# Kernel optimization log

Hardware: AMD Instinct MI355X
Metric: run time of the kernel (lower is better)

Reference implementation:

```python
import jax, jax.numpy as jnp
import numpy as np

B, P, D, A = 256, 196, 512, 512

def setup_inputs() -> dict:
    key = jax.random.key(0)
    ks = jax.random.split(key, 12)
    sc = 1.0 / np.sqrt(D)
    sa = 1.0 / np.sqrt(A)
    return {
        "encoder_out": jax.random.normal(ks[0], (B, P, D), jnp.float32),
        "decoder_hidden": jax.random.normal(ks[1], (B, D), jnp.float32),
        "st": jax.random.normal(ks[2], (B, D), jnp.float32),
        "Wv": jax.random.normal(ks[3], (D, A), jnp.float32) * sc,
        "bv": jnp.zeros((A,), jnp.float32),
        "Wh": jax.random.normal(ks[4], (D, A), jnp.float32) * sc,
        "bh": jnp.zeros((A,), jnp.float32),
        "Ws": jax.random.normal(ks[5], (D, A), jnp.float32) * sc,
        "bs": jnp.zeros((A,), jnp.float32),
        "Wav": jax.random.normal(ks[6], (A,), jnp.float32) * sa,
        "bav": jnp.zeros((), jnp.float32),
        "Was": jax.random.normal(ks[7], (A,), jnp.float32) * sa,
        "bas": jnp.zeros((), jnp.float32),
    }

def reference(encoder_out, decoder_hidden, st, Wv, bv, Wh, bh, Ws, bs, Wav, bav, Was, bas):
    # hidden: (B, A)
    hidden = decoder_hidden @ Wh + bh
    # v: (B, P, A)
    v = jnp.einsum('bpd,da->bpa', encoder_out, Wv) + bv
    # z_t: (B, P) -- additive attention scores over pixels
    z_t = jnp.einsum('bpa,a->bp', jnp.tanh(v + hidden[:, None, :]), Wav) + bav
    alpha_t = jax.nn.softmax(z_t, axis=1)
    # c_t: (B, D) -- attention-weighted encoding
    c_t = jnp.einsum('bpd,bp->bd', encoder_out, alpha_t)
    # sentinel branch: s (B, A), s_att (B, 1)
    s = st @ Ws + bs
    s_att = jnp.tanh(s + hidden) @ Was + bas  # (B,)
    z_t_extended = jnp.concatenate([z_t, s_att[:, None]], axis=1)  # (B, P+1)
    alpha_t_hat = jax.nn.softmax(z_t_extended, axis=1)
    beta_t = alpha_t_hat[:, -1:]  # (B, 1)
    c_hat_t = beta_t * st + (1.0 - beta_t) * c_t
    return (c_hat_t, alpha_t, beta_t)
```

## Files before the change

### kernel.cpp

```cpp
#include <hip/hip_runtime.h>
#include <hip/hip_bf16.h>
#include <cstdint>

#define B_ 256
#define P_ 196
#define D_ 512
#define A_ 512

#define OUT_CHAT  0
#define OUT_ALPHA (B_*D_)
#define OUT_BETA  (B_*D_ + B_*P_)

typedef unsigned short ushort_t;
typedef uint32_t u32;
typedef uint64_t u64;
typedef __attribute__((ext_vector_type(8))) __bf16 bf16x8;
typedef __attribute__((ext_vector_type(4))) float f32x4;

__device__ __forceinline__ ushort_t f2bf(float f) {
    union { float f; u32 i; } v; v.f = f;
    u32 r = (v.i + 0x7fffu + ((v.i >> 16) & 1u)) >> 16;
    return (ushort_t)r;
}
__device__ __forceinline__ float bfbits2f(u32 lo16) {
    union { u32 i; float f; } v; v.i = lo16 << 16; return v.f;
}
__device__ __forceinline__ u32 cvt2bf(float x, float y) {
    union { __hip_bfloat162 h; u32 u; } v;
    v.h = __float22bfloat162_rn(make_float2(x, y));
    return v.u;
}
__device__ __forceinline__ float tanh_fast(float x) {
    float e = __expf(2.0f * x);
    return 1.0f - 2.0f / (e + 1.0f);
}
__device__ __forceinline__ void async_load16(const ushort_t* g, ushort_t* l) {
    __builtin_amdgcn_global_load_lds(
        (const __attribute__((address_space(1))) unsigned int*)g,
        (__attribute__((address_space(3))) unsigned int*)l, 16, 0, 0);
}
__device__ __forceinline__ void fma8(float ap, uint4 v, float ac[8]) {
    ac[0] = fmaf(ap, bfbits2f(v.x & 0xffffu), ac[0]);
    ac[1] = fmaf(ap, bfbits2f(v.x >> 16),     ac[1]);
    ac[2] = fmaf(ap, bfbits2f(v.y & 0xffffu), ac[2]);
    ac[3] = fmaf(ap, bfbits2f(v.y >> 16),     ac[3]);
    ac[4] = fmaf(ap, bfbits2f(v.z & 0xffffu), ac[4]);
    ac[5] = fmaf(ap, bfbits2f(v.z >> 16),     ac[5]);
    ac[6] = fmaf(ap, bfbits2f(v.w & 0xffffu), ac[6]);
    ac[7] = fmaf(ap, bfbits2f(v.w >> 16),     ac[7]);
}

__global__ __launch_bounds__(256) void k_prep(
    const float* __restrict__ E, const float* __restrict__ dh,
    const float* __restrict__ st,
    const float* __restrict__ Wv, const float* __restrict__ Wh,
    const float* __restrict__ Ws,
    ushort_t* __restrict__ Ebf, ushort_t* __restrict__ dhbf,
    ushort_t* __restrict__ stbf,
    ushort_t* __restrict__ WvT, ushort_t* __restrict__ WhT,
    ushort_t* __restrict__ WsT)
{
    __shared__ ushort_t tile[32][33];
    int bx = blockIdx.x;
    if (bx < 12544) {
        size_t i0 = (size_t)bx * 512 + threadIdx.x;
        const float4* src = (const float4*)E;
        u64* dst = (u64*)Ebf;
        float4 v0 = src[i0];
        float4 v1 = src[i0 + 256];
        dst[i0]       = (u64)cvt2bf(v0.x, v0.y) | ((u64)cvt2bf(v0.z, v0.w) << 32);
        dst[i0 + 256] = (u64)cvt2bf(v1.x, v1.y) | ((u64)cvt2bf(v1.z, v1.w) << 32);
    } else if (bx < 12672) {
        int gid = (bx - 12544) * 256 + threadIdx.x;
        float4 dv = ((const float4*)dh)[gid];
        float4 sv = ((const float4*)st)[gid];
        ((u64*)dhbf)[gid] = (u64)cvt2bf(dv.x, dv.y) | ((u64)cvt2bf(dv.z, dv.w) << 32);
        ((u64*)stbf)[gid] = (u64)cvt2bf(sv.x, sv.y) | ((u64)cvt2bf(sv.z, sv.w) << 32);
    } else {
        int idx = bx - 12672;
        int z   = idx >> 8;
        int rem = idx & 255;
        int tby = rem >> 4, tbx = rem & 15;
        const float* W  = (z == 0) ? Wv  : (z == 1) ? Wh  : Ws;
        ushort_t*    WT = (z == 0) ? WvT : (z == 1) ? WhT : WsT;
        int t = threadIdx.x, r = t >> 5, c = t & 31;
#pragma unroll
        for (int i = 0; i < 4; ++i) {
            int row = r + 8 * i;
            tile[row][c] = f2bf(W[(size_t)(tby * 32 + row) * A_ + tbx * 32 + c]);
        }
        __syncthreads();
#pragma unroll
        for (int i = 0; i < 4; ++i) {
            int row = r + 8 * i;
            WT[(size_t)(tbx * 32 + row) * D_ + tby * 32 + c] = tile[c][row];
        }
    }
}

#define PADK 72

__global__ __launch_bounds__(256) void k1_mfma(
    const ushort_t* __restrict__ dhbf, const ushort_t* __restrict__ stbf,
    const ushort_t* __restrict__ WhT,  const ushort_t* __restrict__ WsT,
    const float* __restrict__ bh, const float* __restrict__ bs,
    float* __restrict__ hidden_ws, float* __restrict__ s_ws)
{
    __shared__ ushort_t As[128 * PADK];
    __shared__ ushort_t Bs[128 * PADK];

    int mat = blockIdx.z;
    const ushort_t* Abf = mat ? stbf : dhbf;
    const ushort_t* WT  = mat ? WsT  : WhT;
    const float*    bia = mat ? bs   : bh;
    float*          outp = mat ? s_ws : hidden_ws;

    int tid = threadIdx.x;
    int m0 = blockIdx.y * 128;
    int n0 = blockIdx.x * 128;

    int lane = tid & 63, w = tid >> 6;
    int wm = w & 1, wn = w >> 1;
    int col = lane & 15, q = lane >> 4;

    f32x4 acc[4][4];
#pragma unroll
    for (int tm = 0; tm < 4; ++tm)
#pragma unroll
        for (int tn = 0; tn < 4; ++tn)
            acc[tm][tn] = (f32x4){0.f, 0.f, 0.f, 0.f};

    const ushort_t* arow = As + (wm * 64 + col) * PADK + q * 8;
    const ushort_t* brow = Bs + (wn * 64 + col) * PADK + q * 8;

    int sr = tid >> 3, sc = tid & 7;
    for (int kt = 0; kt < D_ / 64; ++kt) {
#pragma unroll
        for (int i = 0; i < 4; ++i) {
            int row = sr + i * 32;
            *(uint4*)(As + row * PADK + sc * 8) =
                *(const uint4*)(Abf + (size_t)(m0 + row) * D_ + kt * 64 + sc * 8);
            *(uint4*)(Bs + row * PADK + sc * 8) =
                *(const uint4*)(WT + (size_t)(n0 + row) * D_ + kt * 64 + sc * 8);
        }
        __syncthreads();
#pragma unroll
        for (int ks = 0; ks < 2; ++ks) {
            bf16x8 afr[4];
#pragma unroll
            for (int tm = 0; tm < 4; ++tm)
                afr[tm] = *(const bf16x8*)(arow + tm * 16 * PADK + ks * 32);
#pragma unroll
            for (int tn = 0; tn < 4; ++tn) {
                bf16x8 bfr = *(const bf16x8*)(brow + tn * 16 * PADK + ks * 32);
#pragma unroll
                for (int tm = 0; tm < 4; ++tm)
                    acc[tm][tn] = __builtin_amdgcn_mfma_f32_16x16x32_bf16(
                        afr[tm], bfr, acc[tm][tn], 0, 0, 0);
            }
        }
        __syncthreads();
    }

#pragma unroll
    for (int tm = 0; tm < 4; ++tm)
#pragma unroll
        for (int r = 0; r < 4; ++r) {
            int b = m0 + wm * 64 + tm * 16 + q * 4 + r;
#pragma unroll
            for (int tn = 0; tn < 4; ++tn) {
                int n = n0 + wn * 64 + tn * 16 + col;
                outp[(size_t)b * A_ + n] = acc[tm][tn][r] + bia[n];
            }
        }
}

#define BM 128
#define BN 256
#define BKk 64
__global__ __launch_bounds__(256, 3) void k2_z_bf(
    const ushort_t* __restrict__ Ebf, const ushort_t* __restrict__ WvT,
    const float* __restrict__ hidden_ws, const float* __restrict__ bv,
    const float* __restrict__ Wav, float* __restrict__ z2_ws)
{
    __shared__ ushort_t As[BM * BKk];
    __shared__ ushort_t Bs[BN * BKk];
    __shared__ float hv_s[2][BN];
    __shared__ float wav_s[BN];
    __shared__ float zpart[2][BM];

    int tid = threadIdx.x;
    int bx  = blockIdx.x;
    int m_idx = ((bx >> 4) << 3) + (bx & 7);
    int half  = (bx >> 3) & 1;
    int m0  = m_idx * BM;
    int n0  = half * BN;
    int b0  = m0 / P_;
    int b1  = (m0 + BM - 1) / P_;

    {
        int a = n0 + tid;
        float bva = bv[a];
        hv_s[0][tid] = hidden_ws[(size_t)b0 * A_ + a] + bva;
        hv_s[1][tid] = hidden_ws[(size_t)b1 * A_ + a] + bva;
        wav_s[tid]   = Wav[a];
    }

    int lane = tid & 63, w = tid >> 6;
    int wm = w & 1, wn = w >> 1;
    int col = lane & 15, q = lane >> 4;

    f32x4 acc[4][8];
#pragma unroll
    for (int tm = 0; tm < 4; ++tm)
#pragma unroll
        for (int tn = 0; tn < 8; ++tn)
            acc[tm][tn] = (f32x4){0.f, 0.f, 0.f, 0.f};

    int srow = tid >> 3, spos = tid & 7;
    int gch  = spos ^ (srow & 7);
    const ushort_t* agb = Ebf + (size_t)(m0 + srow) * D_ + gch * 8;
    const ushort_t* bgb = WvT + (size_t)(n0 + srow) * D_ + gch * 8;
    ushort_t* alb = As + tid * 8;
    ushort_t* blb = Bs + tid * 8;

    int fx = col & 7;

    for (int kt = 0; kt < D_ / BKk; ++kt) {
#pragma unroll
        for (int i = 0; i < 4; ++i)
            async_load16(agb + (size_t)i * 32 * D_ + kt * BKk, alb + i * 2048);
#pragma unroll
        for (int i = 0; i < 8; ++i)
            async_load16(bgb + (size_t)i * 32 * D_ + kt * BKk, blb + i * 2048);
        __syncthreads();
#pragma unroll
        for (int ks = 0; ks < 2; ++ks) {
            bf16x8 afr[4];
#pragma unroll
            for (int tm = 0; tm < 4; ++tm)
                afr[tm] = *(const bf16x8*)(As + (wm * 64 + tm * 16 + col) * BKk
                                              + (((ks * 4 + q) ^ fx) * 8));
#pragma unroll
            for (int tn = 0; tn < 8; ++tn) {
                bf16x8 bfr = *(const bf16x8*)(Bs + (wn * 128 + tn * 16 + col) * BKk
                                                 + (((ks * 4 + q) ^ fx) * 8));
#pragma unroll
                for (int tm = 0; tm < 4; ++tm)
                    acc[tm][tn] = __builtin_amdgcn_mfma_f32_16x16x32_bf16(
                        afr[tm], bfr, acc[tm][tn], 0, 0, 0);
            }
        }
        __syncthreads();
    }

#pragma unroll
    for (int tm = 0; tm < 4; ++tm) {
#pragma unroll
        for (int r = 0; r < 4; ++r) {
            int row = wm * 64 + tm * 16 + q * 4 + r;
            int m   = m0 + row;
            int bsel = (m / P_) - b0;
            float zr = 0.f;
#pragma unroll
            for (int tn = 0; tn < 8; ++tn) {
                int nl = wn * 128 + tn * 16 + col;
                zr += wav_s[nl] * tanh_fast(acc[tm][tn][r] + hv_s[bsel][nl]);
            }
#pragma unroll
            for (int msk = 1; msk < 16; msk <<= 1)
                zr += __shfl_xor(zr, msk, 64);
            if (col == 0) zpart[wn][row] = zr;
        }
    }
    __syncthreads();
    if (tid < BM)
        z2_ws[(size_t)half * (B_ * P_) + m0 + tid] =
            zpart[0][tid] + zpart[1][tid];
}

__global__ __launch_bounds__(512) void k34_softmax_ct(
    const ushort_t* __restrict__ Ebf, const float* __restrict__ st,
    const float* __restrict__ z2_ws, const float* __restrict__ hidden_ws,
    const float* __restrict__ s_ws, const float* __restrict__ Was,
    const float* __restrict__ bas, const float* __restrict__ bav,
    float* __restrict__ out)
{
    __shared__ float red[8];
    __shared__ float al[P_];
    __shared__ float acc_s[8][516];
    __shared__ float bm_s, bl_s, sa_s;

    int b = blockIdx.x, t = threadIdx.x;
    int lane = t & 63, w = t >> 6;

    float part = Was[t] * tanh_fast(s_ws[(size_t)b * A_ + t]
                                  + hidden_ws[(size_t)b * A_ + t]);
#pragma unroll
    for (int o = 32; o >= 1; o >>= 1) part += __shfl_down(part, o, 64);
    if (lane == 0) red[w] = part;
    __syncthreads();
    if (t == 0) {
        float s = 0.f;
#pragma unroll
        for (int i = 0; i < 8; ++i) s += red[i];
        sa_s = s + bas[0];
    }
    __syncthreads();

    float zv = (t < P_) ? (z2_ws[(size_t)b * P_ + t]
                         + z2_ws[(size_t)(B_ * P_) + (size_t)b * P_ + t] + bav[0])
                        : -1e30f;
    float m = zv;
#pragma unroll
    for (int o = 32; o >= 1; o >>= 1) m = fmaxf(m, __shfl_xor(m, o, 64));
    if (lane == 0) red[w] = m;
    __syncthreads();
    if (t == 0) {
        float mm = red[0];
#pragma unroll
        for (int i = 1; i < 8; ++i) mm = fmaxf(mm, red[i]);
        bm_s = mm;
    }
    __syncthreads();
    float m1 = bm_s;
    float e = (t < P_) ? __expf(zv - m1) : 0.f;
    float s = e;
#pragma unroll
    for (int o = 32; o >= 1; o >>= 1) s += __shfl_xor(s, o, 64);
    if (lane == 0) red[w] = s;
    __syncthreads();
    if (t == 0) {
        float ss = 0.f;
#pragma unroll
        for (int i = 0; i < 8; ++i) ss += red[i];
        bl_s = ss;
    }
    __syncthreads();
    float l1 = bl_s;
    if (t < P_) {
        float alpha = e / l1;
        al[t] = alpha;
        out[OUT_ALPHA + (size_t)b * P_ + t] = alpha;
    }
    float sa = sa_s;
    float m2 = fmaxf(m1, sa);
    float eb2 = __expf(sa - m2);
    float l2 = __expf(m1 - m2) * l1 + eb2;
    float beta = eb2 / l2;
    if (t == 0) out[OUT_BETA + b] = beta;
    __syncthreads();

    float ac[8] = {0.f, 0.f, 0.f, 0.f, 0.f, 0.f, 0.f, 0.f};
    const uint4* eb = (const uint4*)(Ebf + (size_t)b * P_ * D_);
#pragma unroll 4
    for (int i = 0; i < 24; ++i) {
        int pp = w + 8 * i;
        uint4 v = eb[(size_t)pp * (D_ / 8) + lane];
        fma8(al[pp], v, ac);
    }
    if (w < P_ - 192) {
        int pp = 192 + w;
        uint4 v = eb[(size_t)pp * (D_ / 8) + lane];
        fma8(al[pp], v, ac);
    }
#pragma unroll
    for (int j = 0; j < 8; ++j) acc_s[w][lane * 8 + j] = ac[j];
    __syncthreads();
    float c = 0.f;
#pragma unroll
    for (int g = 0; g < 8; ++g) c += acc_s[g][t];
    float sv = st[(size_t)b * D_ + t];
    out[OUT_CHAT + (size_t)b * D_ + t] = beta * sv + (1.f - beta) * c;
}

extern "C" void kernel_launch(void* const* d_in, const int* in_sizes, int n_in,
                              void* d_out, int out_size, void* d_ws, size_t ws_size,
                              hipStream_t stream)
{
    (void)in_sizes; (void)n_in; (void)out_size; (void)ws_size;
    const float* E   = (const float*)d_in[0];
    const float* dh  = (const float*)d_in[1];
    const float* st  = (const float*)d_in[2];
    const float* Wv  = (const float*)d_in[3];
    const float* bv  = (const float*)d_in[4];
    const float* Wh  = (const float*)d_in[5];
    const float* bh  = (const float*)d_in[6];
    const float* Ws  = (const float*)d_in[7];
    const float* bs  = (const float*)d_in[8];
    const float* Wav = (const float*)d_in[9];
    const float* bav = (const float*)d_in[10];
    const float* Was = (const float*)d_in[11];
    const float* bas = (const float*)d_in[12];
    float* out = (float*)d_out;

    char* ws = (char*)d_ws;
    ushort_t* WvT     = (ushort_t*)(ws);
    ushort_t* WhT     = (ushort_t*)(ws + 524288);
    ushort_t* WsT     = (ushort_t*)(ws + 1048576);
    float*    z2_w    = (float*)(ws + 1572864);
    ushort_t* dhbf    = (ushort_t*)(ws + 1974272);
    ushort_t* stbf    = (ushort_t*)(ws + 2236416);
    float*    hidden_w= (float*)(ws + 2498560);
    float*    s_w     = (float*)(ws + 3022848);
    ushort_t* Ebf     = (ushort_t*)(ws + 3547136);

    k_prep<<<12544 + 128 + 768, 256, 0, stream>>>(E, dh, st, Wv, Wh, Ws,
                                                  Ebf, dhbf, stbf, WvT, WhT, WsT);
    k1_mfma<<<dim3(4, 2, 2), 256, 0, stream>>>(dhbf, stbf, WhT, WsT, bh, bs,
                                               hidden_w, s_w);
    k2_z_bf<<<784, 256, 0, stream>>>(Ebf, WvT, hidden_w, bv, Wav, z2_w);
    k34_softmax_ct<<<256, 512, 0, stream>>>(Ebf, st, z2_w, hidden_w, s_w,
                                            Was, bas, bav, out);
}
```

Measured before the change: 251.3 us.

## Double-buffer k2 GEMM tiles, shrink N tile, interleave z partial sums

The score GEMM kernel now double-buffers its A and B shared-memory tiles, so the next K slice is prefetched while the current one is multiplied. The N tile shrinks from 256 to 128, giving a 2D grid of four N-blocks per M tile with fewer accumulators per thread, and occupancy is lowered to 2 blocks per CU. Partial z sums are stored interleaved, four per row, so the softmax kernel reads them with one float4 load. The z workspace now reuses the WhT/WsT region, which is safe only because k1 has finished reading those buffers before k2 runs.

```diff
diff --git a/kernel.cpp b/kernel.cpp
--- a/kernel.cpp
+++ b/kernel.cpp
@@ -176,29 +176,26 @@
 }
 
 #define BM 128
-#define BN 256
+#define BN2 128
 #define BKk 64
-__global__ __launch_bounds__(256, 3) void k2_z_bf(
+__global__ __launch_bounds__(256, 2) void k2_z_bf(
     const ushort_t* __restrict__ Ebf, const ushort_t* __restrict__ WvT,
     const float* __restrict__ hidden_ws, const float* __restrict__ bv,
     const float* __restrict__ Wav, float* __restrict__ z2_ws)
 {
-    __shared__ ushort_t As[BM * BKk];
-    __shared__ ushort_t Bs[BN * BKk];
-    __shared__ float hv_s[2][BN];
-    __shared__ float wav_s[BN];
+    __shared__ ushort_t As[2][BM * BKk];
+    __shared__ ushort_t Bs[2][BN2 * BKk];
+    __shared__ float hv_s[2][BN2];
+    __shared__ float wav_s[BN2];
     __shared__ float zpart[2][BM];
 
     int tid = threadIdx.x;
-    int bx  = blockIdx.x;
-    int m_idx = ((bx >> 4) << 3) + (bx & 7);
-    int half  = (bx >> 3) & 1;
-    int m0  = m_idx * BM;
-    int n0  = half * BN;
+    int m0  = blockIdx.x * BM;
+    int n0  = blockIdx.y * BN2;
     int b0  = m0 / P_;
     int b1  = (m0 + BM - 1) / P_;
 
-    {
+    if (tid < BN2) {
         int a = n0 + tid;
         float bva = bv[a];
         hv_s[0][tid] = hidden_ws[(size_t)b0 * A_ + a] + bva;
@@ -210,40 +207,50 @@
     int wm = w & 1, wn = w >> 1;
     int col = lane & 15, q = lane >> 4;
 
-    f32x4 acc[4][8];
+    f32x4 acc[4][4];
 #pragma unroll
     for (int tm = 0; tm < 4; ++tm)
 #pragma unroll
-        for (int tn = 0; tn < 8; ++tn)
+        for (int tn = 0; tn < 4; ++tn)
             acc[tm][tn] = (f32x4){0.f, 0.f, 0.f, 0.f};
 
     int srow = tid >> 3, spos = tid & 7;
     int gch  = spos ^ (srow & 7);
     const ushort_t* agb = Ebf + (size_t)(m0 + srow) * D_ + gch * 8;
     const ushort_t* bgb = WvT + (size_t)(n0 + srow) * D_ + gch * 8;
-    ushort_t* alb = As + tid * 8;
-    ushort_t* blb = Bs + tid * 8;
 
     int fx = col & 7;
 
+#pragma unroll
+    for (int i = 0; i < 4; ++i) {
+        async_load16(agb + (size_t)i * 32 * D_, &As[0][0] + tid * 8 + i * 2048);
+        async_load16(bgb + (size_t)i * 32 * D_, &Bs[0][0] + tid * 8 + i * 2048);
+    }
+    __syncthreads();
+
     for (int kt = 0; kt < D_ / BKk; ++kt) {
-#pragma unroll
-        for (int i = 0; i < 4; ++i)
-            async_load16(agb + (size_t)i * 32 * D_ + kt * BKk, alb + i * 2048);
-#pragma unroll
-        for (int i = 0; i < 8; ++i)
-            async_load16(bgb + (size_t)i * 32 * D_ + kt * BKk, blb + i * 2048);
-        __syncthreads();
+        int cur = kt & 1;
+        if (kt < D_ / BKk - 1) {
+#pragma unroll
+            for (int i = 0; i < 4; ++i) {
+                async_load16(agb + (size_t)i * 32 * D_ + (kt + 1) * BKk,
+                             &As[cur ^ 1][0] + tid * 8 + i * 2048);
+                async_load16(bgb + (size_t)i * 32 * D_ + (kt + 1) * BKk,
+                             &Bs[cur ^ 1][0] + tid * 8 + i * 2048);
+            }
+        }
+        const ushort_t* Ab = &As[cur][0];
+        const ushort_t* Bb = &Bs[cur][0];
 #pragma unroll
         for (int ks = 0; ks < 2; ++ks) {
             bf16x8 afr[4];
 #pragma unroll
             for (int tm = 0; tm < 4; ++tm)
-                afr[tm] = *(const bf16x8*)(As + (wm * 64 + tm * 16 + col) * BKk
+                afr[tm] = *(const bf16x8*)(Ab + (wm * 64 + tm * 16 + col) * BKk
                                               + (((ks * 4 + q) ^ fx) * 8));
 #pragma unroll
-            for (int tn = 0; tn < 8; ++tn) {
-                bf16x8 bfr = *(const bf16x8*)(Bs + (wn * 128 + tn * 16 + col) * BKk
+            for (int tn = 0; tn < 4; ++tn) {
+                bf16x8 bfr = *(const bf16x8*)(Bb + (wn * 64 + tn * 16 + col) * BKk
                                                  + (((ks * 4 + q) ^ fx) * 8));
 #pragma unroll
                 for (int tm = 0; tm < 4; ++tm)
@@ -263,8 +270,8 @@
             int bsel = (m / P_) - b0;
             float zr = 0.f;
 #pragma unroll
-            for (int tn = 0; tn < 8; ++tn) {
-                int nl = wn * 128 + tn * 16 + col;
+            for (int tn = 0; tn < 4; ++tn) {
+                int nl = wn * 64 + tn * 16 + col;
                 zr += wav_s[nl] * tanh_fast(acc[tm][tn][r] + hv_s[bsel][nl]);
             }
 #pragma unroll
@@ -275,7 +282,7 @@
     }
     __syncthreads();
     if (tid < BM)
-        z2_ws[(size_t)half * (B_ * P_) + m0 + tid] =
+        z2_ws[(size_t)(m0 + tid) * 4 + blockIdx.y] =
             zpart[0][tid] + zpart[1][tid];
 }
 
@@ -308,9 +315,11 @@
     }
     __syncthreads();
 
-    float zv = (t < P_) ? (z2_ws[(size_t)b * P_ + t]
-                         + z2_ws[(size_t)(B_ * P_) + (size_t)b * P_ + t] + bav[0])
-                        : -1e30f;
+    float zv = -1e30f;
+    if (t < P_) {
+        float4 z4 = ((const float4*)z2_ws)[(size_t)b * P_ + t];
+        zv = z4.x + z4.y + z4.z + z4.w + bav[0];
+    }
     float m = zv;
 #pragma unroll
     for (int o = 32; o >= 1; o >>= 1) m = fmaxf(m, __shfl_xor(m, o, 64));
@@ -398,18 +407,19 @@
     ushort_t* WvT     = (ushort_t*)(ws);
     ushort_t* WhT     = (ushort_t*)(ws + 524288);
     ushort_t* WsT     = (ushort_t*)(ws + 1048576);
-    float*    z2_w    = (float*)(ws + 1572864);
-    ushort_t* dhbf    = (ushort_t*)(ws + 1974272);
-    ushort_t* stbf    = (ushort_t*)(ws + 2236416);
-    float*    hidden_w= (float*)(ws + 2498560);
-    float*    s_w     = (float*)(ws + 3022848);
-    ushort_t* Ebf     = (ushort_t*)(ws + 3547136);
+    float*    z2_w    = (float*)(ws + 524288);
+    ushort_t* dhbf    = (ushort_t*)(ws + 1572864);
+    ushort_t* stbf    = (ushort_t*)(ws + 1835008);
+    float*    hidden_w= (float*)(ws + 2097152);
+    float*    s_w     = (float*)(ws + 2621440);
+    ushort_t* Ebf     = (ushort_t*)(ws + 3145728);
 
     k_prep<<<12544 + 128 + 768, 256, 0, stream>>>(E, dh, st, Wv, Wh, Ws,
                                                   Ebf, dhbf, stbf, WvT, WhT, WsT);
     k1_mfma<<<dim3(4, 2, 2), 256, 0, stream>>>(dhbf, stbf, WhT, WsT, bh, bs,
                                                hidden_w, s_w);
-    k2_z_bf<<<784, 256, 0, stream>>>(Ebf, WvT, hidden_w, bv, Wav, z2_w);
+    k2_z_bf<<<dim3((B_ * P_) / BM, A_ / BN2), 256, 0, stream>>>(
+        Ebf, WvT, hidden_w, bv, Wav, z2_w);
     k34_softmax_ct<<<256, 512, 0, stream>>>(Ebf, st, z2_w, hidden_w, s_w,
                                             Was, bas, bav, out);
 }
```

Result: no change. 256.3 us (+2.0%).

## Stage full-K activation tile in LDS and stream Wv from global per warp

Applied to the files above, without the earlier changes.

The attention-score GEMM kernel is restructured so each block owns 64 rows of the flattened (B·P) dimension across all 512 attention columns. The whole K=512 slice of the bf16 encoder tile is loaded into LDS once, with a single barrier. Each warp then reads its 128 Wv columns straight from global/L2 instead of from a shared tile. This drops the per-K-step barriers and the split of z into two halves, so the softmax kernel reads one z buffer. In exchange, every block re-reads the whole of Wv from L2 without LDS reuse. The large LDS footprint also lowers occupancy, and the workspace is repacked so z aliases the already-consumed WhT region.

```diff
diff --git a/kernel.cpp b/kernel.cpp
--- a/kernel.cpp
+++ b/kernel.cpp
@@ -175,40 +175,45 @@
         }
 }
 
-#define BM 128
-#define BN 256
-#define BKk 64
-__global__ __launch_bounds__(256, 3) void k2_z_bf(
+#define BM3 64
+__global__ __launch_bounds__(256, 2) void k2_z_bf(
     const ushort_t* __restrict__ Ebf, const ushort_t* __restrict__ WvT,
     const float* __restrict__ hidden_ws, const float* __restrict__ bv,
-    const float* __restrict__ Wav, float* __restrict__ z2_ws)
+    const float* __restrict__ Wav, float* __restrict__ z_ws)
 {
-    __shared__ ushort_t As[BM * BKk];
-    __shared__ ushort_t Bs[BN * BKk];
-    __shared__ float hv_s[2][BN];
-    __shared__ float wav_s[BN];
-    __shared__ float zpart[2][BM];
+    __shared__ ushort_t As[BM3 * 512];
+    __shared__ float hv_s[2][A_];
+    __shared__ float wav_s[A_];
+    __shared__ float zpart[4][BM3];
 
     int tid = threadIdx.x;
-    int bx  = blockIdx.x;
-    int m_idx = ((bx >> 4) << 3) + (bx & 7);
-    int half  = (bx >> 3) & 1;
-    int m0  = m_idx * BM;
-    int n0  = half * BN;
-    int b0  = m0 / P_;
-    int b1  = (m0 + BM - 1) / P_;
+    int m0 = blockIdx.x * BM3;
+    int b0 = m0 / P_, b1 = (m0 + BM3 - 1) / P_;
+
+#pragma unroll
+    for (int j = 0; j < 2; ++j) {
+        int a = j * 256 + tid;
+        float bva = bv[a];
+        hv_s[0][a] = hidden_ws[(size_t)b0 * A_ + a] + bva;
+        hv_s[1][a] = hidden_ws[(size_t)b1 * A_ + a] + bva;
+        wav_s[a]   = Wav[a];
+    }
+
+    int lane = tid & 63, w = tid >> 6;
+    int col = lane & 15, q = lane >> 4;
 
     {
-        int a = n0 + tid;
-        float bva = bv[a];
-        hv_s[0][tid] = hidden_ws[(size_t)b0 * A_ + a] + bva;
-        hv_s[1][tid] = hidden_ws[(size_t)b1 * A_ + a] + bva;
-        wav_s[tid]   = Wav[a];
-    }
-
-    int lane = tid & 63, w = tid >> 6;
-    int wm = w & 1, wn = w >> 1;
-    int col = lane & 15, q = lane >> 4;
+        int r0 = tid >> 6, sc = tid & 63;
+#pragma unroll
+        for (int i = 0; i < 16; ++i) {
+            int row  = i * 4 + r0;
+            int slot = sc ^ (row & 7);
+            async_load16(Ebf + (size_t)(m0 + row) * D_ + slot * 8,
+                         As + i * 2048 + tid * 8);
+        }
+    }
+    asm volatile("s_waitcnt vmcnt(0)" ::: "memory");
+    __builtin_amdgcn_s_barrier();
 
     f32x4 acc[4][8];
 #pragma unroll
@@ -217,71 +222,53 @@
         for (int tn = 0; tn < 8; ++tn)
             acc[tm][tn] = (f32x4){0.f, 0.f, 0.f, 0.f};
 
-    int srow = tid >> 3, spos = tid & 7;
-    int gch  = spos ^ (srow & 7);
-    const ushort_t* agb = Ebf + (size_t)(m0 + srow) * D_ + gch * 8;
-    const ushort_t* bgb = WvT + (size_t)(n0 + srow) * D_ + gch * 8;
-    ushort_t* alb = As + tid * 8;
-    ushort_t* blb = Bs + tid * 8;
-
     int fx = col & 7;
-
-    for (int kt = 0; kt < D_ / BKk; ++kt) {
-#pragma unroll
-        for (int i = 0; i < 4; ++i)
-            async_load16(agb + (size_t)i * 32 * D_ + kt * BKk, alb + i * 2048);
-#pragma unroll
-        for (int i = 0; i < 8; ++i)
-            async_load16(bgb + (size_t)i * 32 * D_ + kt * BKk, blb + i * 2048);
-        __syncthreads();
-#pragma unroll
-        for (int ks = 0; ks < 2; ++ks) {
-            bf16x8 afr[4];
+    const ushort_t* bgp = WvT + (size_t)(w * 128 + col) * D_ + q * 8;
+
+#pragma unroll
+    for (int k32 = 0; k32 < 16; ++k32) {
+        bf16x8 afr[4];
+#pragma unroll
+        for (int tm = 0; tm < 4; ++tm)
+            afr[tm] = *(const bf16x8*)(As + (tm * 16 + col) * 512
+                                          + (((k32 * 4 + q) ^ fx) * 8));
+#pragma unroll
+        for (int tn = 0; tn < 8; ++tn) {
+            bf16x8 bfr = *(const bf16x8*)(bgp + (size_t)tn * 16 * D_ + k32 * 32);
 #pragma unroll
             for (int tm = 0; tm < 4; ++tm)
-                afr[tm] = *(const bf16x8*)(As + (wm * 64 + tm * 16 + col) * BKk
-                                              + (((ks * 4 + q) ^ fx) * 8));
+                acc[tm][tn] = __builtin_amdgcn_mfma_f32_16x16x32_bf16(
+                    afr[tm], bfr, acc[tm][tn], 0, 0, 0);
+        }
+    }
+
+#pragma unroll
+    for (int tm = 0; tm < 4; ++tm) {
+#pragma unroll
+        for (int r = 0; r < 4; ++r) {
+            int row = tm * 16 + q * 4 + r;
+            int bsel = ((m0 + row) / P_) - b0;
+            float zr = 0.f;
 #pragma unroll
             for (int tn = 0; tn < 8; ++tn) {
-                bf16x8 bfr = *(const bf16x8*)(Bs + (wn * 128 + tn * 16 + col) * BKk
-                                                 + (((ks * 4 + q) ^ fx) * 8));
-#pragma unroll
-                for (int tm = 0; tm < 4; ++tm)
-                    acc[tm][tn] = __builtin_amdgcn_mfma_f32_16x16x32_bf16(
-                        afr[tm], bfr, acc[tm][tn], 0, 0, 0);
-            }
-        }
-        __syncthreads();
-    }
-
-#pragma unroll
-    for (int tm = 0; tm < 4; ++tm) {
-#pragma unroll
-        for (int r = 0; r < 4; ++r) {
-            int row = wm * 64 + tm * 16 + q * 4 + r;
-            int m   = m0 + row;
-            int bsel = (m / P_) - b0;
-            float zr = 0.f;
-#pragma unroll
-            for (int tn = 0; tn < 8; ++tn) {
-                int nl = wn * 128 + tn * 16 + col;
+                int nl = w * 128 + tn * 16 + col;
                 zr += wav_s[nl] * tanh_fast(acc[tm][tn][r] + hv_s[bsel][nl]);
             }
 #pragma unroll
             for (int msk = 1; msk < 16; msk <<= 1)
                 zr += __shfl_xor(zr, msk, 64);
-            if (col == 0) zpart[wn][row] = zr;
-        }
-    }
-    __syncthreads();
-    if (tid < BM)
-        z2_ws[(size_t)half * (B_ * P_) + m0 + tid] =
-            zpart[0][tid] + zpart[1][tid];
+            if (col == 0) zpart[w][row] = zr;
+        }
+    }
+    __syncthreads();
+    if (tid < BM3)
+        z_ws[m0 + tid] = zpart[0][tid] + zpart[1][tid]
+                       + zpart[2][tid] + zpart[3][tid];
 }
 
 __global__ __launch_bounds__(512) void k34_softmax_ct(
     const ushort_t* __restrict__ Ebf, const float* __restrict__ st,
-    const float* __restrict__ z2_ws, const float* __restrict__ hidden_ws,
+    const float* __restrict__ z_ws, const float* __restrict__ hidden_ws,
     const float* __restrict__ s_ws, const float* __restrict__ Was,
     const float* __restrict__ bas, const float* __restrict__ bav,
     float* __restrict__ out)
@@ -308,9 +295,7 @@
     }
     __syncthreads();
 
-    float zv = (t < P_) ? (z2_ws[(size_t)b * P_ + t]
-                         + z2_ws[(size_t)(B_ * P_) + (size_t)b * P_ + t] + bav[0])
-                        : -1e30f;
+    float zv = (t < P_) ? (z_ws[(size_t)b * P_ + t] + bav[0]) : -1e30f;
     float m = zv;
 #pragma unroll
     for (int o = 32; o >= 1; o >>= 1) m = fmaxf(m, __shfl_xor(m, o, 64));
@@ -398,18 +383,19 @@
     ushort_t* WvT     = (ushort_t*)(ws);
     ushort_t* WhT     = (ushort_t*)(ws + 524288);
     ushort_t* WsT     = (ushort_t*)(ws + 1048576);
-    float*    z2_w    = (float*)(ws + 1572864);
-    ushort_t* dhbf    = (ushort_t*)(ws + 1974272);
-    ushort_t* stbf    = (ushort_t*)(ws + 2236416);
-    float*    hidden_w= (float*)(ws + 2498560);
-    float*    s_w     = (float*)(ws + 3022848);
-    ushort_t* Ebf     = (ushort_t*)(ws + 3547136);
+    float*    z_w     = (float*)(ws + 524288);
+    ushort_t* dhbf    = (ushort_t*)(ws + 1572864);
+    ushort_t* stbf    = (ushort_t*)(ws + 1835008);
+    float*    hidden_w= (float*)(ws + 2097152);
+    float*    s_w     = (float*)(ws + 2621440);
+    ushort_t* Ebf     = (ushort_t*)(ws + 3145728);
 
     k_prep<<<12544 + 128 + 768, 256, 0, stream>>>(E, dh, st, Wv, Wh, Ws,
                                                   Ebf, dhbf, stbf, WvT, WhT, WsT);
     k1_mfma<<<dim3(4, 2, 2), 256, 0, stream>>>(dhbf, stbf, WhT, WsT, bh, bs,
                                                hidden_w, s_w);
-    k2_z_bf<<<784, 256, 0, stream>>>(Ebf, WvT, hidden_w, bv, Wav, z2_w);
-    k34_softmax_ct<<<256, 512, 0, stream>>>(Ebf, st, z2_w, hidden_w, s_w,
+    k2_z_bf<<<(B_ * P_) / BM3, 256, 0, stream>>>(
+        Ebf, WvT, hidden_w, bv, Wav, z_w);
+    k34_softmax_ct<<<256, 512, 0, stream>>>(Ebf, st, z_w, hidden_w, s_w,
                                             Was, bas, bav, out);
 }
```

Result: slower. 289.3 us (+15.1%).
